# Optimization experiments

Measured on AMD Instinct MI355X. Metric: run time of the kernel, lower is better.

## Reference

```python
import jax, jax.numpy as jnp
import numpy as np

N, E, G = 100000, 3200000, 128
F, H = 9, 64


def _lin(key, fan_in, fan_out):
    s = 1.0 / np.sqrt(fan_in)
    k1, k2 = jax.random.split(key)
    W = jax.random.uniform(k1, (fan_in, fan_out), minval=-s, maxval=s, dtype=jnp.float32)
    b = jax.random.uniform(k2, (fan_out,), minval=-s, maxval=s, dtype=jnp.float32)
    return W, b


def setup_inputs() -> dict:
    key = jax.random.key(0)
    ks = jax.random.split(key, 16)
    x = jax.random.normal(ks[0], (N, F), dtype=jnp.float32)
    edge_index = jax.random.randint(ks[1], (2, E), 0, N, dtype=jnp.int64)
    edge_attr = jax.random.normal(ks[2], (E, 1), dtype=jnp.float32)
    batch = jnp.sort(jax.random.randint(ks[3], (N,), 0, G, dtype=jnp.int64))
    B_total = jax.random.uniform(ks[4], (G,), dtype=jnp.float32)
    terminal_mask = jax.random.randint(ks[5], (N,), 0, 2, dtype=jnp.int32)
    c_cost = jax.random.uniform(ks[6], (N,), dtype=jnp.float32)
    We1, be1 = _lin(ks[7], 1, F)   # GINEConv edge projection edge_dim->in_channels
    W1a, b1a = _lin(ks[8], F, H)
    W1b, b1b = _lin(ks[9], H, H)
    We2, be2 = _lin(ks[10], 1, H)
    W2a, b2a = _lin(ks[11], H, H)
    W2b, b2b = _lin(ks[12], H, H)
    Wr1, br1 = _lin(ks[13], H, H // 2)
    Wr2, br2 = _lin(ks[14], H // 2, 1)
    return dict(x=x, edge_index=edge_index, edge_attr=edge_attr, batch=batch,
                B_total=B_total, terminal_mask=terminal_mask, c_cost=c_cost,
                We1=We1, be1=be1, W1a=W1a, b1a=b1a, W1b=W1b, b1b=b1b,
                We2=We2, be2=be2, W2a=W2a, b2a=b2a, W2b=W2b, b2b=b2b,
                Wr1=Wr1, br1=br1, Wr2=Wr2, br2=br2)


def _gine_conv(h, src, dst, edge_attr, We, be, Wa, ba, Wb, bb):
    # GINEConv (eps=0): nn((1+eps)*x_i + sum_j ReLU(x_j + Lin(edge_attr)))
    ea = edge_attr @ We + be                      # [E, dim]
    msg = jax.nn.relu(h[src] + ea)                # gather + edge fuse + relu
    agg = jax.ops.segment_sum(msg, dst, num_segments=N)  # scatter-add
    z = h + agg
    z = jax.nn.relu(z @ Wa + ba)
    return jax.nn.relu(z @ Wb + bb)


def reference(x, edge_index, edge_attr, batch, B_total, terminal_mask, c_cost,
              We1, be1, W1a, b1a, W1b, b1b, We2, be2, W2a, b2a, W2b, b2b,
              Wr1, br1, Wr2, br2):
    src, dst = edge_index[0], edge_index[1]
    h = _gine_conv(x, src, dst, edge_attr, We1, be1, W1a, b1a, W1b, b1b)
    h = _gine_conv(h, src, dst, edge_attr, We2, be2, W2a, b2a, W2b, b2b)
    pi_raw = jax.nn.sigmoid(jax.nn.relu(h @ Wr1 + br1) @ Wr2 + br2)[:, 0]  # [N]
    pi_raw = pi_raw * (1.0 - terminal_mask.astype(pi_raw.dtype))
    node_expenses = pi_raw * c_cost
    total_expenses = jax.ops.segment_sum(node_expenses, batch, num_segments=B_total.shape[0])
    ratio = jnp.minimum(B_total[batch] / (total_expenses[batch] + 1e-12), 1.0)
    return pi_raw * ratio
```

## Files before the change

### kernel.cpp

```cpp
#include <hip/hip_runtime.h>
#include <hip/hip_fp16.h>
#include <math.h>

#define TPB 256
#define P_BLOCKS 512
#define BSHIFT 8
#define BINS_MAX 512

struct alignas(8)  h2x2 { __half2 a, b; };
struct alignas(16) h2x4 { __half2 a, b, c, d; };

__global__ void __launch_bounds__(256) k_bhist(const int* __restrict__ dst,
                                               int* __restrict__ counts, int E, int B) {
  __shared__ int h[BINS_MAX];
  int t = threadIdx.x, blk = blockIdx.x;
  for (int i = t; i < B; i += TPB) h[i] = 0;
  __syncthreads();
  int chunk = (E + P_BLOCKS - 1) / P_BLOCKS;
  int s = blk * chunk, e = min(E, s + chunk);
  for (int i = s + t; i < e; i += TPB)
    atomicAdd(&h[__builtin_nontemporal_load(&dst[i]) >> BSHIFT], 1);
  __syncthreads();
  for (int i = t; i < B; i += TPB) counts[i * P_BLOCKS + blk] = h[i];
}

__global__ void k_scan_block(const int* __restrict__ deg, int* __restrict__ offs,
                             int* __restrict__ bsums, int n) {
  __shared__ int lds[256];
  int t = threadIdx.x, b = blockIdx.x;
  int base = b * 1024 + t * 4;
  int v0 = (base + 0 < n) ? deg[base + 0] : 0;
  int v1 = (base + 1 < n) ? deg[base + 1] : 0;
  int v2 = (base + 2 < n) ? deg[base + 2] : 0;
  int v3 = (base + 3 < n) ? deg[base + 3] : 0;
  int s = v0 + v1 + v2 + v3;
  lds[t] = s;
  __syncthreads();
  int acc = s;
  for (int off = 1; off < 256; off <<= 1) {
    int x = (t >= off) ? lds[t - off] : 0;
    __syncthreads();
    acc += x;
    lds[t] = acc;
    __syncthreads();
  }
  int excl = acc - s;
  if (base + 0 < n) offs[base + 0] = excl;
  if (base + 1 < n) offs[base + 1] = excl + v0;
  if (base + 2 < n) offs[base + 2] = excl + v0 + v1;
  if (base + 3 < n) offs[base + 3] = excl + v0 + v1 + v2;
  if (t == 255) bsums[b] = acc;
}

__global__ void k_scan_mid(int* __restrict__ bsums, int nb) {
  __shared__ int lds[256];
  int t = threadIdx.x;
  int v = (t < nb) ? bsums[t] : 0;
  lds[t] = v;
  __syncthreads();
  int acc = v;
  for (int off = 1; off < 256; off <<= 1) {
    int x = (t >= off) ? lds[t - off] : 0;
    __syncthreads();
    acc += x;
    lds[t] = acc;
    __syncthreads();
  }
  if (t < nb) bsums[t] = acc - v;
}

__global__ void k_scan_add(int* __restrict__ offs, const int* __restrict__ bsums,
                           int n, int total) {
  int t = threadIdx.x, b = blockIdx.x;
  int add = bsums[b];
  int base = b * 1024 + t * 4;
#pragma unroll
  for (int j = 0; j < 4; ++j)
    if (base + j < n) offs[base + j] += add;
  if (b == 0 && t == 0) offs[n] = total;
}

__global__ void __launch_bounds__(256) k_bfill(const int* __restrict__ src,
                                               const int* __restrict__ dst,
                                               const float* __restrict__ attr,
                                               const int* __restrict__ offs,
                                               int2* __restrict__ ebuf, int E, int B) {
  __shared__ int cur[BINS_MAX];
  int t = threadIdx.x, blk = blockIdx.x;
  for (int i = t; i < B; i += TPB) cur[i] = offs[i * P_BLOCKS + blk];
  __syncthreads();
  int chunk = (E + P_BLOCKS - 1) / P_BLOCKS;
  int s = blk * chunk, e = min(E, s + chunk);
#pragma unroll 4
  for (int i = s + t; i < e; i += TPB) {
    int d = __builtin_nontemporal_load(&dst[i]);
    int sv = __builtin_nontemporal_load(&src[i]);
    float av = __builtin_nontemporal_load(&attr[i]);
    int bin = d >> BSHIFT;
    int pos = atomicAdd(&cur[bin], 1);
    ebuf[pos] = make_int2((sv << BSHIFT) | (d & ((1 << BSHIFT) - 1)), __float_as_int(av));
  }
}

__global__ void __launch_bounds__(256) k_bsort(const long long* __restrict__ ebuf,
                                               const int* __restrict__ offs,
                                               int2* __restrict__ csr,
                                               int* __restrict__ noffs,
                                               int N, int E) {
  __shared__ int hist[256];
  __shared__ int cursor[256];
  __shared__ int sc[256];
  int t = threadIdx.x, bkt = blockIdx.x;
  hist[t] = 0;
  __syncthreads();
  int s = offs[bkt * P_BLOCKS], e = offs[(bkt + 1) * P_BLOCKS];
#pragma unroll 4
  for (int i = s + t; i < e; i += TPB) {
    long long pv = __builtin_nontemporal_load(&ebuf[i]);
    int key = (int)(unsigned int)(pv & 0xffffffffLL);
    atomicAdd(&hist[key & 255], 1);
  }
  __syncthreads();
  int v = hist[t];
  int acc = v;
  sc[t] = v;
  __syncthreads();
  for (int off = 1; off < 256; off <<= 1) {
    int x = (t >= off) ? sc[t - off] : 0;
    __syncthreads();
    acc += x;
    sc[t] = acc;
    __syncthreads();
  }
  int base = s + acc - v;
  cursor[t] = base;
  int n = (bkt << BSHIFT) + t;
  if (n < N) noffs[n] = base;
  if (bkt == 0 && t == 0) noffs[N] = E;
  __syncthreads();
#pragma unroll 4
  for (int i = s + t; i < e; i += TPB) {
    long long pv = __builtin_nontemporal_load(&ebuf[i]);
    int key = (int)(unsigned int)(pv & 0xffffffffLL);
    int attr = (int)(unsigned int)(((unsigned long long)pv) >> 32);
    int pos = atomicAdd(&cursor[key & 255], 1);
    csr[pos] = make_int2(((unsigned int)key) >> BSHIFT, attr);
  }
}

__global__ void __launch_bounds__(256) k_agg1(
    const float* __restrict__ x, const int2* __restrict__ csr,
    const int* __restrict__ noffs, const float* __restrict__ We1,
    const float* __restrict__ be1, float* __restrict__ u1, int N) {
  int t = blockIdx.x * TPB + threadIdx.x;
  int node = t >> 4, f = t & 15;
  if (node >= N || f >= 9) return;
  int o0 = noffs[node], o1 = noffs[node + 1];
  float we = We1[f], be = be1[f];
  float acc = 0.f;
  int e = o0;
  for (; e + 3 < o1; e += 4) {
    int2 p0 = csr[e], p1 = csr[e + 1], p2 = csr[e + 2], p3 = csr[e + 3];
    float v0 = x[p0.x * 9 + f] + fmaf(__int_as_float(p0.y), we, be);
    float v1 = x[p1.x * 9 + f] + fmaf(__int_as_float(p1.y), we, be);
    float v2 = x[p2.x * 9 + f] + fmaf(__int_as_float(p2.y), we, be);
    float v3 = x[p3.x * 9 + f] + fmaf(__int_as_float(p3.y), we, be);
    acc += fmaxf(v0, 0.f) + fmaxf(v1, 0.f) + fmaxf(v2, 0.f) + fmaxf(v3, 0.f);
  }
  for (; e < o1; ++e) {
    int2 p = csr[e];
    acc += fmaxf(x[p.x * 9 + f] + fmaf(__int_as_float(p.y), we, be), 0.f);
  }
  u1[node * 9 + f] = x[node * 9 + f] + acc;
}

__global__ void __launch_bounds__(256) k_agg2(
    const __half* __restrict__ h1, const long long* __restrict__ csr,
    const int* __restrict__ noffs, const float* __restrict__ We2,
    const float* __restrict__ be2, float* __restrict__ u2, int N) {
  int gt = blockIdx.x * TPB + threadIdx.x;
  int node = gt >> 6;
  if (node >= N) return;
  int lane = gt & 63;
  int q = lane >> 3, c = lane & 7;
  float4 weA = *(const float4*)&We2[c * 8];
  float4 weB = *(const float4*)&We2[c * 8 + 4];
  float4 beA = *(const float4*)&be2[c * 8];
  float4 beB = *(const float4*)&be2[c * 8 + 4];
  int o0 = noffs[node], o1 = noffs[node + 1];
  float a0 = 0.f, a1 = 0.f, a2 = 0.f, a3 = 0.f, a4 = 0.f, a5 = 0.f, a6 = 0.f, a7 = 0.f;

#define AGG2_ACC(pv, v)                                                      \
  {                                                                          \
    float ea = __int_as_float((int)(unsigned int)(((unsigned long long)(pv)) >> 32)); \
    float2 f0 = __half22float2((v).a), f1 = __half22float2((v).b);           \
    float2 f2 = __half22float2((v).c), f3 = __half22float2((v).d);           \
    a0 += fmaxf(f0.x + fmaf(ea, weA.x, beA.x), 0.f);                         \
    a1 += fmaxf(f0.y + fmaf(ea, weA.y, beA.y), 0.f);                         \
    a2 += fmaxf(f1.x + fmaf(ea, weA.z, beA.z), 0.f);                         \
    a3 += fmaxf(f1.y + fmaf(ea, weA.w, beA.w), 0.f);                         \
    a4 += fmaxf(f2.x + fmaf(ea, weB.x, beB.x), 0.f);                         \
    a5 += fmaxf(f2.y + fmaf(ea, weB.y, beB.y), 0.f);                         \
    a6 += fmaxf(f3.x + fmaf(ea, weB.z, beB.z), 0.f);                         \
    a7 += fmaxf(f3.y + fmaf(ea, weB.w, beB.w), 0.f);                         \
  }

#define AGG2_ACCM(pv, v, m)                                                  \
  {                                                                          \
    float ea = __int_as_float((int)(unsigned int)(((unsigned long long)(pv)) >> 32)); \
    float2 f0 = __half22float2((v).a), f1 = __half22float2((v).b);           \
    float2 f2 = __half22float2((v).c), f3 = __half22float2((v).d);           \
    a0 += (m) ? fmaxf(f0.x + fmaf(ea, weA.x, beA.x), 0.f) : 0.f;             \
    a1 += (m) ? fmaxf(f0.y + fmaf(ea, weA.y, beA.y), 0.f) : 0.f;             \
    a2 += (m) ? fmaxf(f1.x + fmaf(ea, weA.z, beA.z), 0.f) : 0.f;             \
    a3 += (m) ? fmaxf(f1.y + fmaf(ea, weA.w, beA.w), 0.f) : 0.f;             \
    a4 += (m) ? fmaxf(f2.x + fmaf(ea, weB.x, beB.x), 0.f) : 0.f;             \
    a5 += (m) ? fmaxf(f2.y + fmaf(ea, weB.y, beB.y), 0.f) : 0.f;             \
    a6 += (m) ? fmaxf(f3.x + fmaf(ea, weB.z, beB.z), 0.f) : 0.f;             \
    a7 += (m) ? fmaxf(f3.y + fmaf(ea, weB.w, beB.w), 0.f) : 0.f;             \
  }

  int e = o0;
  for (; e + 32 <= o1; e += 32) {
    long long pv0 = __builtin_nontemporal_load(&csr[e + q]);
    long long pv1 = __builtin_nontemporal_load(&csr[e + 8 + q]);
    long long pv2 = __builtin_nontemporal_load(&csr[e + 16 + q]);
    long long pv3 = __builtin_nontemporal_load(&csr[e + 24 + q]);
    h2x4 v0 = *(const h2x4*)(h1 + (size_t)(int)(unsigned int)(pv0 & 0xffffffffLL) * 64 + c * 8);
    h2x4 v1 = *(const h2x4*)(h1 + (size_t)(int)(unsigned int)(pv1 & 0xffffffffLL) * 64 + c * 8);
    h2x4 v2 = *(const h2x4*)(h1 + (size_t)(int)(unsigned int)(pv2 & 0xffffffffLL) * 64 + c * 8);
    h2x4 v3 = *(const h2x4*)(h1 + (size_t)(int)(unsigned int)(pv3 & 0xffffffffLL) * 64 + c * 8);
    AGG2_ACC(pv0, v0); AGG2_ACC(pv1, v1); AGG2_ACC(pv2, v2); AGG2_ACC(pv3, v3);
  }
  if (e < o1) {
    int last = o1 - 1;
    int i0 = e + q;      bool m0 = i0 < o1; i0 = m0 ? i0 : last;
    int i1 = e + 8 + q;  bool m1 = i1 < o1; i1 = m1 ? i1 : last;
    int i2 = e + 16 + q; bool m2 = i2 < o1; i2 = m2 ? i2 : last;
    int i3 = e + 24 + q; bool m3 = i3 < o1; i3 = m3 ? i3 : last;
    long long pv0 = __builtin_nontemporal_load(&csr[i0]);
    long long pv1 = __builtin_nontemporal_load(&csr[i1]);
    long long pv2 = __builtin_nontemporal_load(&csr[i2]);
    long long pv3 = __builtin_nontemporal_load(&csr[i3]);
    h2x4 v0 = *(const h2x4*)(h1 + (size_t)(int)(unsigned int)(pv0 & 0xffffffffLL) * 64 + c * 8);
    h2x4 v1 = *(const h2x4*)(h1 + (size_t)(int)(unsigned int)(pv1 & 0xffffffffLL) * 64 + c * 8);
    h2x4 v2 = *(const h2x4*)(h1 + (size_t)(int)(unsigned int)(pv2 & 0xffffffffLL) * 64 + c * 8);
    h2x4 v3 = *(const h2x4*)(h1 + (size_t)(int)(unsigned int)(pv3 & 0xffffffffLL) * 64 + c * 8);
    AGG2_ACCM(pv0, v0, m0); AGG2_ACCM(pv1, v1, m1);
    AGG2_ACCM(pv2, v2, m2); AGG2_ACCM(pv3, v3, m3);
  }
#undef AGG2_ACC
#undef AGG2_ACCM

  a0 += __shfl_xor(a0, 8, 64); a0 += __shfl_xor(a0, 16, 64); a0 += __shfl_xor(a0, 32, 64);
  a1 += __shfl_xor(a1, 8, 64); a1 += __shfl_xor(a1, 16, 64); a1 += __shfl_xor(a1, 32, 64);
  a2 += __shfl_xor(a2, 8, 64); a2 += __shfl_xor(a2, 16, 64); a2 += __shfl_xor(a2, 32, 64);
  a3 += __shfl_xor(a3, 8, 64); a3 += __shfl_xor(a3, 16, 64); a3 += __shfl_xor(a3, 32, 64);
  a4 += __shfl_xor(a4, 8, 64); a4 += __shfl_xor(a4, 16, 64); a4 += __shfl_xor(a4, 32, 64);
  a5 += __shfl_xor(a5, 8, 64); a5 += __shfl_xor(a5, 16, 64); a5 += __shfl_xor(a5, 32, 64);
  a6 += __shfl_xor(a6, 8, 64); a6 += __shfl_xor(a6, 16, 64); a6 += __shfl_xor(a6, 32, 64);
  a7 += __shfl_xor(a7, 8, 64); a7 += __shfl_xor(a7, 16, 64); a7 += __shfl_xor(a7, 32, 64);

  if (q == 0) {
    h2x4 sf = *(const h2x4*)(h1 + (size_t)node * 64 + c * 8);
    float2 s0 = __half22float2(sf.a), s1 = __half22float2(sf.b);
    float2 s2 = __half22float2(sf.c), s3 = __half22float2(sf.d);
    float4 oA, oB;
    oA.x = s0.x + a0; oA.y = s0.y + a1; oA.z = s1.x + a2; oA.w = s1.y + a3;
    oB.x = s2.x + a4; oB.y = s2.y + a5; oB.z = s3.x + a6; oB.w = s3.y + a7;
    *(float4*)&u2[(size_t)node * 64 + c * 8] = oA;
    *(float4*)&u2[(size_t)node * 64 + c * 8 + 4] = oB;
  }
}

__global__ void __launch_bounds__(256) k_mlp9(
    const float* __restrict__ uin, const float* __restrict__ Wa,
    const float* __restrict__ ba, const float* __restrict__ Wb,
    const float* __restrict__ bb, __half* __restrict__ hout, int N) {
  constexpr int KIN = 9;
  __shared__ float ls_in[64 * KIN];
  __shared__ float ls_z[64 * 65];
  __shared__ float ls_w[64 * 64];
  __shared__ float ls_b[128];
  const int t = threadIdx.x;
  const int n0 = blockIdx.x * 64;

  for (int i = t; i < 64 * KIN; i += TPB) {
    int r = i / KIN, c = i % KIN;
    int g = n0 + r;
    ls_in[i] = (g < N) ? uin[g * KIN + c] : 0.f;
  }
  for (int i = t; i < KIN * 64; i += TPB) ls_w[i] = Wa[i];
  if (t < 64) { ls_b[t] = ba[t]; ls_b[64 + t] = bb[t]; }
  __syncthreads();

  const int of = (t & 15) * 4, nb = (t >> 4) * 4;
  float acc[4][4];
#pragma unroll
  for (int i = 0; i < 4; ++i)
#pragma unroll
    for (int j = 0; j < 4; ++j) acc[i][j] = 0.f;

  for (int k = 0; k < KIN; ++k) {
    float4 w = *(const float4*)&ls_w[k * 64 + of];
#pragma unroll
    for (int ni = 0; ni < 4; ++ni) {
      float uv = ls_in[(nb + ni) * KIN + k];
      acc[ni][0] += uv * w.x; acc[ni][1] += uv * w.y;
      acc[ni][2] += uv * w.z; acc[ni][3] += uv * w.w;
    }
  }
#pragma unroll
  for (int ni = 0; ni < 4; ++ni)
#pragma unroll
    for (int oi = 0; oi < 4; ++oi)
      ls_z[(nb + ni) * 65 + of + oi] = fmaxf(acc[ni][oi] + ls_b[of + oi], 0.f);
  __syncthreads();
  for (int i = t; i < 4096; i += TPB) ls_w[i] = Wb[i];
  __syncthreads();

#pragma unroll
  for (int i = 0; i < 4; ++i)
#pragma unroll
    for (int j = 0; j < 4; ++j) acc[i][j] = 0.f;
  for (int k = 0; k < 64; ++k) {
    float4 w = *(const float4*)&ls_w[k * 64 + of];
#pragma unroll
    for (int ni = 0; ni < 4; ++ni) {
      float zv = ls_z[(nb + ni) * 65 + k];
      acc[ni][0] += zv * w.x; acc[ni][1] += zv * w.y;
      acc[ni][2] += zv * w.z; acc[ni][3] += zv * w.w;
    }
  }
#pragma unroll
  for (int ni = 0; ni < 4; ++ni) {
    int n = n0 + nb + ni;
    if (n < N) {
      float ox = fmaxf(acc[ni][0] + ls_b[64 + of + 0], 0.f);
      float oy = fmaxf(acc[ni][1] + ls_b[64 + of + 1], 0.f);
      float oz = fmaxf(acc[ni][2] + ls_b[64 + of + 2], 0.f);
      float ow = fmaxf(acc[ni][3] + ls_b[64 + of + 3], 0.f);
      h2x2 hv;
      hv.a = __float22half2_rn(make_float2(ox, oy));
      hv.b = __float22half2_rn(make_float2(oz, ow));
      *(h2x2*)(hout + (size_t)n * 64 + of) = hv;
    }
  }
}

__global__ void __launch_bounds__(256) k_mlp_ro(
    const float* __restrict__ uin, const float* __restrict__ Wa,
    const float* __restrict__ ba, const float* __restrict__ Wb,
    const float* __restrict__ bb, const float* __restrict__ Wr1,
    const float* __restrict__ br1, const float* __restrict__ Wr2,
    const float* __restrict__ br2, const int* __restrict__ tmask,
    float* __restrict__ pi, int N) {
  __shared__ float ls_in[64 * 65];
  __shared__ float ls_z[64 * 65];
  __shared__ float ls_w[64 * 64];
  __shared__ float ls_b[128];
  __shared__ float ls_w2[32];
  __shared__ float ls_b1[32];
  const int t = threadIdx.x;
  const int n0 = blockIdx.x * 64;

  for (int i = t; i < 64 * 64; i += TPB) {
    int r = i >> 6, c = i & 63;
    int g = n0 + r;
    ls_in[r * 65 + c] = (g < N) ? uin[(size_t)g * 64 + c] : 0.f;
  }
  for (int i = t; i < 4096; i += TPB) ls_w[i] = Wa[i];
  if (t < 64) { ls_b[t] = ba[t]; ls_b[64 + t] = bb[t]; }
  __syncthreads();

  const int of = (t & 15) * 4, nb = (t >> 4) * 4;
  float acc[4][4];
#pragma unroll
  for (int i = 0; i < 4; ++i)
#pragma unroll
    for (int j = 0; j < 4; ++j) acc[i][j] = 0.f;
  for (int k = 0; k < 64; ++k) {
    float4 w = *(const float4*)&ls_w[k * 64 + of];
#pragma unroll
    for (int ni = 0; ni < 4; ++ni) {
      float uv = ls_in[(nb + ni) * 65 + k];
      acc[ni][0] += uv * w.x; acc[ni][1] += uv * w.y;
      acc[ni][2] += uv * w.z; acc[ni][3] += uv * w.w;
    }
  }
#pragma unroll
  for (int ni = 0; ni < 4; ++ni)
#pragma unroll
    for (int oi = 0; oi < 4; ++oi)
      ls_z[(nb + ni) * 65 + of + oi] = fmaxf(acc[ni][oi] + ls_b[of + oi], 0.f);
  __syncthreads();
  for (int i = t; i < 4096; i += TPB) ls_w[i] = Wb[i];
  __syncthreads();

#pragma unroll
  for (int i = 0; i < 4; ++i)
#pragma unroll
    for (int j = 0; j < 4; ++j) acc[i][j] = 0.f;
  for (int k = 0; k < 64; ++k) {
    float4 w = *(const float4*)&ls_w[k * 64 + of];
#pragma unroll
    for (int ni = 0; ni < 4; ++ni) {
      float zv = ls_z[(nb + ni) * 65 + k];
      acc[ni][0] += zv * w.x; acc[ni][1] += zv * w.y;
      acc[ni][2] += zv * w.z; acc[ni][3] += zv * w.w;
    }
  }
#pragma unroll
  for (int ni = 0; ni < 4; ++ni)
#pragma unroll
    for (int oi = 0; oi < 4; ++oi)
      ls_in[(nb + ni) * 65 + of + oi] = fmaxf(acc[ni][oi] + ls_b[64 + of + oi], 0.f);
  __syncthreads();
  for (int i = t; i < 2048; i += TPB) ls_w[i] = Wr1[i];
  if (t < 32) { ls_w2[t] = Wr2[t]; ls_b1[t] = br1[t]; }
  __syncthreads();

  int of32 = t & 31, q8 = t >> 5;
  float b2 = br2[0];
#pragma unroll
  for (int j = 0; j < 8; ++j) {
    int n = q8 * 8 + j;
    float a = 0.f;
    for (int k = 0; k < 64; ++k) a += ls_in[n * 65 + k] * ls_w[k * 32 + of32];
    float r = fmaxf(a + ls_b1[of32], 0.f) * ls_w2[of32];
    for (int s = 16; s > 0; s >>= 1) r += __shfl_down(r, s, 32);
    if (of32 == 0) {
      int g = n0 + n;
      if (g < N) {
        float sg = 1.f / (1.f + expf(-(r + b2)));
        pi[g] = sg * (1.f - (float)tmask[g]);
      }
    }
  }
}

__global__ void k_grpsum(const float* __restrict__ pi, const float* __restrict__ c_cost,
                         const int* __restrict__ batch, float* __restrict__ exp_tot, int N) {
  __shared__ float lsf[256];
  __shared__ int lsi[256];
  int t = threadIdx.x;
  int i = blockIdx.x * TPB + t;
  bool valid = i < N;
  int g = valid ? batch[i] : 0;
  float v = valid ? pi[i] * c_cost[i] : 0.f;
  lsi[t] = valid ? g : 0x7fffffff;
  __syncthreads();
  for (int s = 128; s > 0; s >>= 1) { if (t < s) lsi[t] = min(lsi[t], lsi[t + s]); __syncthreads(); }
  int gmin = lsi[0];
  __syncthreads();
  lsi[t] = valid ? g : -1;
  __syncthreads();
  for (int s = 128; s > 0; s >>= 1) { if (t < s) lsi[t] = max(lsi[t], lsi[t + s]); __syncthreads(); }
  int gmax = lsi[0];
  __syncthreads();
  for (int gg = gmin; gg <= gmax; ++gg) {
    lsf[t] = (valid && g == gg) ? v : 0.f;
    __syncthreads();
    for (int s = 128; s > 0; s >>= 1) { if (t < s) lsf[t] += lsf[t + s]; __syncthreads(); }
    if (t == 0) atomicAdd(&exp_tot[gg], lsf[0]);
    __syncthreads();
  }
}

__global__ void k_final(const float* __restrict__ pi, const int* __restrict__ batch,
                        const float* __restrict__ B_total, const float* __restrict__ exp_tot,
                        float* __restrict__ out, int N) {
  int i = blockIdx.x * TPB + threadIdx.x;
  if (i < N) {
    int g = batch[i];
    float ratio = fminf(B_total[g] / (exp_tot[g] + 1e-12f), 1.f);
    out[i] = pi[i] * ratio;
  }
}

extern "C" void kernel_launch(void* const* d_in, const int* in_sizes, int n_in,
                              void* d_out, int out_size, void* d_ws, size_t ws_size,
                              hipStream_t stream) {
  const float* x     = (const float*)d_in[0];
  const int*   ei    = (const int*)d_in[1];
  const float* eattr = (const float*)d_in[2];
  const int*   batch = (const int*)d_in[3];
  const float* Btot  = (const float*)d_in[4];
  const int*   tmask = (const int*)d_in[5];
  const float* ccost = (const float*)d_in[6];
  const float* We1 = (const float*)d_in[7],  *be1 = (const float*)d_in[8];
  const float* W1a = (const float*)d_in[9],  *b1a = (const float*)d_in[10];
  const float* W1b = (const float*)d_in[11], *b1b = (const float*)d_in[12];
  const float* We2 = (const float*)d_in[13], *be2 = (const float*)d_in[14];
  const float* W2a = (const float*)d_in[15], *b2a = (const float*)d_in[16];
  const float* W2b = (const float*)d_in[17], *b2b = (const float*)d_in[18];
  const float* Wr1 = (const float*)d_in[19], *br1 = (const float*)d_in[20];
  const float* Wr2 = (const float*)d_in[21], *br2 = (const float*)d_in[22];
  float* out = (float*)d_out;

  const int N = in_sizes[0] / 9;
  const int E = in_sizes[2];
  const int G = in_sizes[4];
  const int* src = ei;
  const int* dst = ei + E;
  const int B = (N + (1 << BSHIFT) - 1) >> BSHIFT;
  const int nscan = B * P_BLOCKS;

  size_t cur = 0;
  auto alloc = [&](size_t elems) { size_t r = cur; cur += elems; cur = (cur + 63) & ~(size_t)63; return r; };
  char* wsb = (char*)d_ws;
  size_t o_exp    = alloc(G);
  size_t o_counts = alloc(nscan);
  size_t o_offs   = alloc(nscan + 1);
  size_t o_bsums  = alloc(256);
  size_t o_noffs  = alloc(N + 1);
  size_t o_csr    = alloc(2 * (size_t)E);
  size_t e_or_h   = (2 * (size_t)E > (size_t)N * 32) ? 2 * (size_t)E : (size_t)N * 32;
  size_t o_ebuf   = alloc(e_or_h);
  size_t o_u1     = alloc((size_t)N * 9);
  size_t o_u2     = alloc((size_t)N * 64);
  size_t o_pi     = alloc(N);
  (void)ws_size;

  float* exp_t  = (float*)wsb + o_exp;
  int*   counts = (int*)wsb + o_counts;
  int*   offs   = (int*)wsb + o_offs;
  int*   bsums  = (int*)wsb + o_bsums;
  int*   noffs  = (int*)wsb + o_noffs;
  int2*  csr    = (int2*)((int*)wsb + o_csr);
  int2*  ebuf   = (int2*)((int*)wsb + o_ebuf);
  __half* h1h   = (__half*)((int*)wsb + o_ebuf);
  float* u1     = (float*)wsb + o_u1;
  float* u2     = (float*)wsb + o_u2;
  float* pi     = (float*)wsb + o_pi;

  (void)hipMemsetAsync(exp_t, 0, (size_t)G * 4, stream);

  const int nb = (nscan + 1023) / 1024;

  k_bhist<<<P_BLOCKS, TPB, 0, stream>>>(dst, counts, E, B);
  k_scan_block<<<nb, TPB, 0, stream>>>(counts, offs, bsums, nscan);
  k_scan_mid<<<1, 256, 0, stream>>>(bsums, nb);
  k_scan_add<<<nb, TPB, 0, stream>>>(offs, bsums, nscan, E);
  k_bfill<<<P_BLOCKS, TPB, 0, stream>>>(src, dst, eattr, offs, ebuf, E, B);
  k_bsort<<<B, TPB, 0, stream>>>((const long long*)ebuf, offs, csr, noffs, N, E);

  k_agg1<<<((size_t)N * 16 + TPB - 1) / TPB, TPB, 0, stream>>>(x, csr, noffs, We1, be1, u1, N);
  k_mlp9<<<(N + 63) / 64, TPB, 0, stream>>>(u1, W1a, b1a, W1b, b1b, h1h, N);

  k_agg2<<<((size_t)N * 64 + TPB - 1) / TPB, TPB, 0, stream>>>(h1h, (const long long*)csr, noffs, We2, be2, u2, N);
  k_mlp_ro<<<(N + 63) / 64, TPB, 0, stream>>>(u2, W2a, b2a, W2b, b2b, Wr1, br1, Wr2, br2, tmask, pi, N);

  k_grpsum<<<(N + TPB - 1) / TPB, TPB, 0, stream>>>(pi, ccost, batch, exp_t, N);
  k_final<<<(N + TPB - 1) / TPB, TPB, 0, stream>>>(pi, batch, Btot, exp_t, out, N);
}
```

Baseline: 472.2 us.

## Pad layer-1 features to 16 floats and aggregate with a wavefront per node

Adds a prep kernel that copies x into a 16-float padded layout and builds padded edge weight/bias vectors. Layer-1 aggregation now gives each node a 64-lane wavefront: 16 edges are processed in parallel with float4 gathers, and the partial sums are reduced with shuffles. The old version used 16 threads per node with 9 active, each walking every edge serially with scalar strided loads. In exchange it adds an extra kernel launch and padded-copy traffic, and it reuses the u2 and ebuf workspace as temporaries.

```diff
diff --git a/kernel.cpp b/kernel.cpp
--- a/kernel.cpp
+++ b/kernel.cpp
@@ -148,30 +148,97 @@
   }
 }
 
+__global__ void __launch_bounds__(256) k_prep(const float* __restrict__ x,
+                                              const float* __restrict__ We1,
+                                              const float* __restrict__ be1,
+                                              float* __restrict__ x16,
+                                              float* __restrict__ wpad, int N) {
+  int i = blockIdx.x * TPB + threadIdx.x;
+  if (i < 32) {
+    int f = i & 15;
+    wpad[i] = (f < 9) ? ((i < 16) ? We1[f] : be1[f]) : 0.f;
+  }
+  int total = N * 16;
+  for (int j = i; j < total; j += gridDim.x * TPB) {
+    int n = j >> 4, f = j & 15;
+    x16[j] = (f < 9) ? x[n * 9 + f] : 0.f;
+  }
+}
+
 __global__ void __launch_bounds__(256) k_agg1(
-    const float* __restrict__ x, const int2* __restrict__ csr,
-    const int* __restrict__ noffs, const float* __restrict__ We1,
-    const float* __restrict__ be1, float* __restrict__ u1, int N) {
-  int t = blockIdx.x * TPB + threadIdx.x;
-  int node = t >> 4, f = t & 15;
-  if (node >= N || f >= 9) return;
+    const float* __restrict__ x16, const long long* __restrict__ csr,
+    const int* __restrict__ noffs, const float* __restrict__ wpad,
+    float* __restrict__ u1, int N) {
+  int gt = blockIdx.x * TPB + threadIdx.x;
+  int node = gt >> 6;
+  if (node >= N) return;
+  int lane = gt & 63;
+  int q = lane >> 2, c = lane & 3;
+  float4 we = *(const float4*)&wpad[c * 4];
+  float4 be = *(const float4*)&wpad[16 + c * 4];
   int o0 = noffs[node], o1 = noffs[node + 1];
-  float we = We1[f], be = be1[f];
-  float acc = 0.f;
+  float a0 = 0.f, a1 = 0.f, a2 = 0.f, a3 = 0.f;
+
+#define AGG1_ACC(pv, v)                                                       \
+  {                                                                           \
+    float ea = __int_as_float((int)(unsigned int)(((unsigned long long)(pv)) >> 32)); \
+    a0 += fmaxf((v).x + fmaf(ea, we.x, be.x), 0.f);                           \
+    a1 += fmaxf((v).y + fmaf(ea, we.y, be.y), 0.f);                           \
+    a2 += fmaxf((v).z + fmaf(ea, we.z, be.z), 0.f);                           \
+    a3 += fmaxf((v).w + fmaf(ea, we.w, be.w), 0.f);                           \
+  }
+#define AGG1_ACCM(pv, v, m)                                                   \
+  {                                                                           \
+    float ea = __int_as_float((int)(unsigned int)(((unsigned long long)(pv)) >> 32)); \
+    a0 += (m) ? fmaxf((v).x + fmaf(ea, we.x, be.x), 0.f) : 0.f;               \
+    a1 += (m) ? fmaxf((v).y + fmaf(ea, we.y, be.y), 0.f) : 0.f;               \
+    a2 += (m) ? fmaxf((v).z + fmaf(ea, we.z, be.z), 0.f) : 0.f;               \
+    a3 += (m) ? fmaxf((v).w + fmaf(ea, we.w, be.w), 0.f) : 0.f;               \
+  }
+
   int e = o0;
-  for (; e + 3 < o1; e += 4) {
-    int2 p0 = csr[e], p1 = csr[e + 1], p2 = csr[e + 2], p3 = csr[e + 3];
-    float v0 = x[p0.x * 9 + f] + fmaf(__int_as_float(p0.y), we, be);
-    float v1 = x[p1.x * 9 + f] + fmaf(__int_as_float(p1.y), we, be);
-    float v2 = x[p2.x * 9 + f] + fmaf(__int_as_float(p2.y), we, be);
-    float v3 = x[p3.x * 9 + f] + fmaf(__int_as_float(p3.y), we, be);
-    acc += fmaxf(v0, 0.f) + fmaxf(v1, 0.f) + fmaxf(v2, 0.f) + fmaxf(v3, 0.f);
-  }
-  for (; e < o1; ++e) {
-    int2 p = csr[e];
-    acc += fmaxf(x[p.x * 9 + f] + fmaf(__int_as_float(p.y), we, be), 0.f);
-  }
-  u1[node * 9 + f] = x[node * 9 + f] + acc;
+  for (; e + 64 <= o1; e += 64) {
+    long long pv0 = csr[e + q];
+    long long pv1 = csr[e + 16 + q];
+    long long pv2 = csr[e + 32 + q];
+    long long pv3 = csr[e + 48 + q];
+    float4 v0 = *(const float4*)(x16 + (size_t)(int)(unsigned int)(pv0 & 0xffffffffLL) * 16 + c * 4);
+    float4 v1 = *(const float4*)(x16 + (size_t)(int)(unsigned int)(pv1 & 0xffffffffLL) * 16 + c * 4);
+    float4 v2 = *(const float4*)(x16 + (size_t)(int)(unsigned int)(pv2 & 0xffffffffLL) * 16 + c * 4);
+    float4 v3 = *(const float4*)(x16 + (size_t)(int)(unsigned int)(pv3 & 0xffffffffLL) * 16 + c * 4);
+    AGG1_ACC(pv0, v0); AGG1_ACC(pv1, v1); AGG1_ACC(pv2, v2); AGG1_ACC(pv3, v3);
+  }
+  if (e < o1) {
+    int last = o1 - 1;
+    int i0 = e + q;      bool m0 = i0 < o1; i0 = m0 ? i0 : last;
+    int i1 = e + 16 + q; bool m1 = i1 < o1; i1 = m1 ? i1 : last;
+    int i2 = e + 32 + q; bool m2 = i2 < o1; i2 = m2 ? i2 : last;
+    int i3 = e + 48 + q; bool m3 = i3 < o1; i3 = m3 ? i3 : last;
+    long long pv0 = csr[i0];
+    long long pv1 = csr[i1];
+    long long pv2 = csr[i2];
+    long long pv3 = csr[i3];
+    float4 v0 = *(const float4*)(x16 + (size_t)(int)(unsigned int)(pv0 & 0xffffffffLL) * 16 + c * 4);
+    float4 v1 = *(const float4*)(x16 + (size_t)(int)(unsigned int)(pv1 & 0xffffffffLL) * 16 + c * 4);
+    float4 v2 = *(const float4*)(x16 + (size_t)(int)(unsigned int)(pv2 & 0xffffffffLL) * 16 + c * 4);
+    float4 v3 = *(const float4*)(x16 + (size_t)(int)(unsigned int)(pv3 & 0xffffffffLL) * 16 + c * 4);
+    AGG1_ACCM(pv0, v0, m0); AGG1_ACCM(pv1, v1, m1);
+    AGG1_ACCM(pv2, v2, m2); AGG1_ACCM(pv3, v3, m3);
+  }
+#undef AGG1_ACC
+#undef AGG1_ACCM
+
+  a0 += __shfl_xor(a0, 4, 64); a0 += __shfl_xor(a0, 8, 64); a0 += __shfl_xor(a0, 16, 64); a0 += __shfl_xor(a0, 32, 64);
+  a1 += __shfl_xor(a1, 4, 64); a1 += __shfl_xor(a1, 8, 64); a1 += __shfl_xor(a1, 16, 64); a1 += __shfl_xor(a1, 32, 64);
+  a2 += __shfl_xor(a2, 4, 64); a2 += __shfl_xor(a2, 8, 64); a2 += __shfl_xor(a2, 16, 64); a2 += __shfl_xor(a2, 32, 64);
+  a3 += __shfl_xor(a3, 4, 64); a3 += __shfl_xor(a3, 8, 64); a3 += __shfl_xor(a3, 16, 64); a3 += __shfl_xor(a3, 32, 64);
+
+  if (q == 0) {
+    float4 sf = *(const float4*)(x16 + (size_t)node * 16 + c * 4);
+    float4 o;
+    o.x = sf.x + a0; o.y = sf.y + a1; o.z = sf.z + a2; o.w = sf.w + a3;
+    *(float4*)&u1[(size_t)node * 16 + c * 4] = o;
+  }
 }
 
 __global__ void __launch_bounds__(256) k_agg2(
@@ -288,7 +355,7 @@
   for (int i = t; i < 64 * KIN; i += TPB) {
     int r = i / KIN, c = i % KIN;
     int g = n0 + r;
-    ls_in[i] = (g < N) ? uin[g * KIN + c] : 0.f;
+    ls_in[i] = (g < N) ? uin[(size_t)g * 16 + c] : 0.f;
   }
   for (int i = t; i < KIN * 64; i += TPB) ls_w[i] = Wa[i];
   if (t < 64) { ls_b[t] = ba[t]; ls_b[64 + t] = bb[t]; }
@@ -514,10 +581,11 @@
   size_t o_offs   = alloc(nscan + 1);
   size_t o_bsums  = alloc(256);
   size_t o_noffs  = alloc(N + 1);
+  size_t o_wpad   = alloc(64);
   size_t o_csr    = alloc(2 * (size_t)E);
-  size_t e_or_h   = (2 * (size_t)E > (size_t)N * 32) ? 2 * (size_t)E : (size_t)N * 32;
+  size_t need_hx  = (size_t)N * 48;
+  size_t e_or_h   = (2 * (size_t)E > need_hx) ? 2 * (size_t)E : need_hx;
   size_t o_ebuf   = alloc(e_or_h);
-  size_t o_u1     = alloc((size_t)N * 9);
   size_t o_u2     = alloc((size_t)N * 64);
   size_t o_pi     = alloc(N);
   (void)ws_size;
@@ -527,11 +595,13 @@
   int*   offs   = (int*)wsb + o_offs;
   int*   bsums  = (int*)wsb + o_bsums;
   int*   noffs  = (int*)wsb + o_noffs;
+  float* wpad   = (float*)wsb + o_wpad;
   int2*  csr    = (int2*)((int*)wsb + o_csr);
   int2*  ebuf   = (int2*)((int*)wsb + o_ebuf);
   __half* h1h   = (__half*)((int*)wsb + o_ebuf);
-  float* u1     = (float*)wsb + o_u1;
+  float* x16    = (float*)((int*)wsb + o_ebuf + (size_t)N * 32);
   float* u2     = (float*)wsb + o_u2;
+  float* u1p    = u2;
   float* pi     = (float*)wsb + o_pi;
 
   (void)hipMemsetAsync(exp_t, 0, (size_t)G * 4, stream);
@@ -545,8 +615,10 @@
   k_bfill<<<P_BLOCKS, TPB, 0, stream>>>(src, dst, eattr, offs, ebuf, E, B);
   k_bsort<<<B, TPB, 0, stream>>>((const long long*)ebuf, offs, csr, noffs, N, E);
 
-  k_agg1<<<((size_t)N * 16 + TPB - 1) / TPB, TPB, 0, stream>>>(x, csr, noffs, We1, be1, u1, N);
-  k_mlp9<<<(N + 63) / 64, TPB, 0, stream>>>(u1, W1a, b1a, W1b, b1b, h1h, N);
+  k_prep<<<2048, TPB, 0, stream>>>(x, We1, be1, x16, wpad, N);
+
+  k_agg1<<<((size_t)N * 64 + TPB - 1) / TPB, TPB, 0, stream>>>(x16, (const long long*)csr, noffs, wpad, u1p, N);
+  k_mlp9<<<(N + 63) / 64, TPB, 0, stream>>>(u1p, W1a, b1a, W1b, b1b, h1h, N);
 
   k_agg2<<<((size_t)N * 64 + TPB - 1) / TPB, TPB, 0, stream>>>(h1h, (const long long*)csr, noffs, We2, be2, u2, N);
   k_mlp_ro<<<(N + 63) / 64, TPB, 0, stream>>>(u2, W2a, b2a, W2b, b2b, Wr1, br1, Wr2, br2, tmask, pi, N);
```

New measurement: 478.4 us. About the same (+1.3%).

## Use split-fp16 MFMA for the layer-2 MLP and readout

Applied to the files above, without the earlier changes.

Rewrites the final MLP and readout kernel to run its three matrix multiplies on MFMA 16x16x32 fp16 instructions instead of scalar FMA loops. Each fp32 operand is split into a high and a low fp16 part, and three MFMAs per tile keep the result close to fp32 accuracy. Weights are repacked into shared memory in the MFMA operand layout, and inputs are loaded straight into registers. The readout reduction now uses lane shuffles across the MFMA output layout. This adds per-block weight packing work and some precision risk. It targets only one of several kernels, so its share of total time may be small.

```diff
diff --git a/kernel.cpp b/kernel.cpp
--- a/kernel.cpp
+++ b/kernel.cpp
@@ -9,6 +9,12 @@
 
 struct alignas(8)  h2x2 { __half2 a, b; };
 struct alignas(16) h2x4 { __half2 a, b, c, d; };
+
+typedef _Float16 f16;
+typedef __attribute__((ext_vector_type(8))) _Float16 f16x8;
+typedef __attribute__((ext_vector_type(4))) float f32x4;
+
+#define MFMA16(a, b, c) __builtin_amdgcn_mfma_f32_16x16x32_f16(a, b, c, 0, 0, 0)
 
 __global__ void __launch_bounds__(256) k_bhist(const int* __restrict__ dst,
                                                int* __restrict__ counts, int E, int B) {
@@ -348,6 +354,35 @@
   }
 }
 
+__device__ __forceinline__ void splitf8(const float* v, f16x8& h, f16x8& l) {
+#pragma unroll
+  for (int j = 0; j < 8; ++j) {
+    float x = v[j];
+    f16 hh = (f16)x;
+    h[j] = hh;
+    l[j] = (f16)(x - (float)hh);
+  }
+}
+
+__device__ __forceinline__ void pack_w(const float* __restrict__ W, int Ntiles, int nslots,
+                                       f16* hi, f16* lo, int t) {
+  int lane = t & 63;
+  int kg = lane >> 4, m = lane & 15;
+  int Nout = Ntiles * 16;
+  for (int s = t >> 6; s < nslots; s += 4) {
+    int ks = s / Ntiles, nt = s - ks * Ntiles;
+    int kbase = ks * 32 + kg * 8;
+    int n = nt * 16 + m;
+    float v[8];
+#pragma unroll
+    for (int j = 0; j < 8; ++j) v[j] = W[(kbase + j) * Nout + n];
+    f16x8 h, l;
+    splitf8(v, h, l);
+    *(f16x8*)&hi[(s * 64 + lane) * 8] = h;
+    *(f16x8*)&lo[(s * 64 + lane) * 8] = l;
+  }
+}
+
 __global__ void __launch_bounds__(256) k_mlp_ro(
     const float* __restrict__ uin, const float* __restrict__ Wa,
     const float* __restrict__ ba, const float* __restrict__ Wb,
@@ -355,85 +390,138 @@
     const float* __restrict__ br1, const float* __restrict__ Wr2,
     const float* __restrict__ br2, const int* __restrict__ tmask,
     float* __restrict__ pi, int N) {
-  __shared__ float ls_in[64 * 65];
+  __shared__ __align__(16) f16 wf1h[4096], wf1l[4096];
+  __shared__ __align__(16) f16 wf2h[4096], wf2l[4096];
+  __shared__ __align__(16) f16 wfrh[2048], wfrl[2048];
   __shared__ float ls_z[64 * 65];
-  __shared__ float ls_w[64 * 64];
-  __shared__ float ls_b[128];
-  __shared__ float ls_w2[32];
-  __shared__ float ls_b1[32];
+  __shared__ float ls_ba[64], ls_bb[64], ls_br1[32], ls_w2[32];
   const int t = threadIdx.x;
   const int n0 = blockIdx.x * 64;
 
-  for (int i = t; i < 64 * 64; i += TPB) {
-    int r = i >> 6, c = i & 63;
-    int g = n0 + r;
-    ls_in[r * 65 + c] = (g < N) ? uin[(size_t)g * 64 + c] : 0.f;
-  }
-  for (int i = t; i < 4096; i += TPB) ls_w[i] = Wa[i];
-  if (t < 64) { ls_b[t] = ba[t]; ls_b[64 + t] = bb[t]; }
-  __syncthreads();
-
-  const int of = (t & 15) * 4, nb = (t >> 4) * 4;
-  float acc[4][4];
-#pragma unroll
-  for (int i = 0; i < 4; ++i)
-#pragma unroll
-    for (int j = 0; j < 4; ++j) acc[i][j] = 0.f;
-  for (int k = 0; k < 64; ++k) {
-    float4 w = *(const float4*)&ls_w[k * 64 + of];
-#pragma unroll
-    for (int ni = 0; ni < 4; ++ni) {
-      float uv = ls_in[(nb + ni) * 65 + k];
-      acc[ni][0] += uv * w.x; acc[ni][1] += uv * w.y;
-      acc[ni][2] += uv * w.z; acc[ni][3] += uv * w.w;
-    }
-  }
-#pragma unroll
-  for (int ni = 0; ni < 4; ++ni)
-#pragma unroll
-    for (int oi = 0; oi < 4; ++oi)
-      ls_z[(nb + ni) * 65 + of + oi] = fmaxf(acc[ni][oi] + ls_b[of + oi], 0.f);
-  __syncthreads();
-  for (int i = t; i < 4096; i += TPB) ls_w[i] = Wb[i];
-  __syncthreads();
-
-#pragma unroll
-  for (int i = 0; i < 4; ++i)
-#pragma unroll
-    for (int j = 0; j < 4; ++j) acc[i][j] = 0.f;
-  for (int k = 0; k < 64; ++k) {
-    float4 w = *(const float4*)&ls_w[k * 64 + of];
-#pragma unroll
-    for (int ni = 0; ni < 4; ++ni) {
-      float zv = ls_z[(nb + ni) * 65 + k];
-      acc[ni][0] += zv * w.x; acc[ni][1] += zv * w.y;
-      acc[ni][2] += zv * w.z; acc[ni][3] += zv * w.w;
-    }
-  }
-#pragma unroll
-  for (int ni = 0; ni < 4; ++ni)
-#pragma unroll
-    for (int oi = 0; oi < 4; ++oi)
-      ls_in[(nb + ni) * 65 + of + oi] = fmaxf(acc[ni][oi] + ls_b[64 + of + oi], 0.f);
-  __syncthreads();
-  for (int i = t; i < 2048; i += TPB) ls_w[i] = Wr1[i];
-  if (t < 32) { ls_w2[t] = Wr2[t]; ls_b1[t] = br1[t]; }
-  __syncthreads();
-
-  int of32 = t & 31, q8 = t >> 5;
+  pack_w(Wa, 4, 8, wf1h, wf1l, t);
+  pack_w(Wb, 4, 8, wf2h, wf2l, t);
+  pack_w(Wr1, 2, 4, wfrh, wfrl, t);
+  if (t < 64) { ls_ba[t] = ba[t]; ls_bb[t] = bb[t]; }
+  else if (t < 96) { ls_br1[t - 64] = br1[t - 64]; ls_w2[t - 64] = Wr2[t - 64]; }
+  __syncthreads();
+
+  const int w = t >> 6, lane = t & 63;
+  const int m = lane & 15, kg = lane >> 4;
+
+  int row = n0 + w * 16 + m;
+  row = min(row, N - 1);
+  const float* ar = uin + (size_t)row * 64 + kg * 8;
+  float av0[8], av1[8];
+  {
+    f32x4 p0 = *(const f32x4*)ar;
+    f32x4 p1 = *(const f32x4*)(ar + 4);
+    f32x4 p2 = *(const f32x4*)(ar + 32);
+    f32x4 p3 = *(const f32x4*)(ar + 36);
+#pragma unroll
+    for (int j = 0; j < 4; ++j) {
+      av0[j] = p0[j]; av0[4 + j] = p1[j];
+      av1[j] = p2[j]; av1[4 + j] = p3[j];
+    }
+  }
+  f16x8 a0h, a0l, a1h, a1l;
+  splitf8(av0, a0h, a0l);
+  splitf8(av1, a1h, a1l);
+
+  f32x4 acc[4];
+#pragma unroll
+  for (int nt = 0; nt < 4; ++nt) { f32x4 z4 = {0.f, 0.f, 0.f, 0.f}; acc[nt] = z4; }
+#pragma unroll
+  for (int nt = 0; nt < 4; ++nt) {
+#pragma unroll
+    for (int ks = 0; ks < 2; ++ks) {
+      int s = ks * 4 + nt;
+      f16x8 bh = *(const f16x8*)&wf1h[(s * 64 + lane) * 8];
+      f16x8 bl = *(const f16x8*)&wf1l[(s * 64 + lane) * 8];
+      f16x8 ah = ks ? a1h : a0h;
+      f16x8 al = ks ? a1l : a0l;
+      acc[nt] = MFMA16(ah, bh, acc[nt]);
+      acc[nt] = MFMA16(al, bh, acc[nt]);
+      acc[nt] = MFMA16(ah, bl, acc[nt]);
+    }
+  }
+#pragma unroll
+  for (int nt = 0; nt < 4; ++nt)
+#pragma unroll
+    for (int r = 0; r < 4; ++r)
+      ls_z[(w * 16 + kg * 4 + r) * 65 + nt * 16 + m] = fmaxf(acc[nt][r] + ls_ba[nt * 16 + m], 0.f);
+  __syncthreads();
+
+  const float* zr = &ls_z[(size_t)(w * 16 + m) * 65 + kg * 8];
+  {
+    float zv0[8], zv1[8];
+#pragma unroll
+    for (int j = 0; j < 8; ++j) { zv0[j] = zr[j]; zv1[j] = zr[32 + j]; }
+    splitf8(zv0, a0h, a0l);
+    splitf8(zv1, a1h, a1l);
+  }
+#pragma unroll
+  for (int nt = 0; nt < 4; ++nt) { f32x4 z4 = {0.f, 0.f, 0.f, 0.f}; acc[nt] = z4; }
+#pragma unroll
+  for (int nt = 0; nt < 4; ++nt) {
+#pragma unroll
+    for (int ks = 0; ks < 2; ++ks) {
+      int s = ks * 4 + nt;
+      f16x8 bh = *(const f16x8*)&wf2h[(s * 64 + lane) * 8];
+      f16x8 bl = *(const f16x8*)&wf2l[(s * 64 + lane) * 8];
+      f16x8 ah = ks ? a1h : a0h;
+      f16x8 al = ks ? a1l : a0l;
+      acc[nt] = MFMA16(ah, bh, acc[nt]);
+      acc[nt] = MFMA16(al, bh, acc[nt]);
+      acc[nt] = MFMA16(ah, bl, acc[nt]);
+    }
+  }
+  __syncthreads();
+#pragma unroll
+  for (int nt = 0; nt < 4; ++nt)
+#pragma unroll
+    for (int r = 0; r < 4; ++r)
+      ls_z[(w * 16 + kg * 4 + r) * 65 + nt * 16 + m] = fmaxf(acc[nt][r] + ls_bb[nt * 16 + m], 0.f);
+  __syncthreads();
+
+  {
+    float zv0[8], zv1[8];
+#pragma unroll
+    for (int j = 0; j < 8; ++j) { zv0[j] = zr[j]; zv1[j] = zr[32 + j]; }
+    splitf8(zv0, a0h, a0l);
+    splitf8(zv1, a1h, a1l);
+  }
+  f32x4 accr[2];
+#pragma unroll
+  for (int nt = 0; nt < 2; ++nt) { f32x4 z4 = {0.f, 0.f, 0.f, 0.f}; accr[nt] = z4; }
+#pragma unroll
+  for (int nt = 0; nt < 2; ++nt) {
+#pragma unroll
+    for (int ks = 0; ks < 2; ++ks) {
+      int s = ks * 2 + nt;
+      f16x8 bh = *(const f16x8*)&wfrh[(s * 64 + lane) * 8];
+      f16x8 bl = *(const f16x8*)&wfrl[(s * 64 + lane) * 8];
+      f16x8 ah = ks ? a1h : a0h;
+      f16x8 al = ks ? a1l : a0l;
+      accr[nt] = MFMA16(ah, bh, accr[nt]);
+      accr[nt] = MFMA16(al, bh, accr[nt]);
+      accr[nt] = MFMA16(ah, bl, accr[nt]);
+    }
+  }
   float b2 = br2[0];
 #pragma unroll
-  for (int j = 0; j < 8; ++j) {
-    int n = q8 * 8 + j;
-    float a = 0.f;
-    for (int k = 0; k < 64; ++k) a += ls_in[n * 65 + k] * ls_w[k * 32 + of32];
-    float r = fmaxf(a + ls_b1[of32], 0.f) * ls_w2[of32];
-    for (int s = 16; s > 0; s >>= 1) r += __shfl_down(r, s, 32);
-    if (of32 == 0) {
-      int g = n0 + n;
-      if (g < N) {
-        float sg = 1.f / (1.f + expf(-(r + b2)));
-        pi[g] = sg * (1.f - (float)tmask[g]);
+  for (int r = 0; r < 4; ++r) {
+    float v0 = fmaxf(accr[0][r] + ls_br1[m], 0.f) * ls_w2[m];
+    float v1 = fmaxf(accr[1][r] + ls_br1[16 + m], 0.f) * ls_w2[16 + m];
+    float tr = v0 + v1;
+    tr += __shfl_xor(tr, 1, 64);
+    tr += __shfl_xor(tr, 2, 64);
+    tr += __shfl_xor(tr, 4, 64);
+    tr += __shfl_xor(tr, 8, 64);
+    if (m == 0) {
+      int node = n0 + w * 16 + kg * 4 + r;
+      if (node < N) {
+        float sg = 1.f / (1.f + expf(-(tr + b2)));
+        pi[node] = sg * (1.f - (float)tmask[node]);
       }
     }
   }
```

Result: faster. 425.8 us (-9.8%).
